# Kernel optimization log

Measured on AMD Instinct MI355X. Metric: run time of the kernel, lower is better.

The kernel has to match this reference:

```python
import jax, jax.numpy as jnp
import numpy as np

B, R, S, H = 4, 64, 512, 768
E = 64            # candidate entities per example
SEG = 128         # seg_emb_dim
NT, NC, NP = 6, 13, 3
REP = 3 * H + 2 * SEG  # rel_rep_size = 2560
NEG = -1e30


def setup_inputs() -> dict:
    key = jax.random.key(0)
    ks = jax.random.split(key, 12)
    hidden_states = jax.random.normal(ks[0], (B, S, H), dtype=jnp.float32)
    rel_pairs = jax.random.randint(ks[1], (B, R, 2), 0, E, dtype=jnp.int64)
    rel_masks = jax.random.randint(ks[2], (B, R, S), 0, 2, dtype=jnp.int32)
    rel_sizes = jax.random.randint(ks[3], (B, R, 2), 0, 30, dtype=jnp.int64)
    ent_span_reps = jax.random.normal(ks[4], (B, E, H), dtype=jnp.float32)
    ent_segs_embs = jax.random.normal(ks[5], (B, E, SEG), dtype=jnp.float32)
    s = 1.0 / np.sqrt(REP)
    W_type = jax.random.uniform(ks[6], (REP, NT), jnp.float32, -s, s)
    b_type = jax.random.uniform(ks[7], (NT,), jnp.float32, -s, s)
    W_cate = jax.random.uniform(ks[8], (REP, NC), jnp.float32, -s, s)
    b_cate = jax.random.uniform(ks[9], (NC,), jnp.float32, -s, s)
    W_pola = jax.random.uniform(ks[10], (REP, NP), jnp.float32, -s, s)
    b_pola = jax.random.uniform(ks[11], (NP,), jnp.float32, -s, s)
    return {"hidden_states": hidden_states, "rel_pairs": rel_pairs,
            "rel_masks": rel_masks, "rel_sizes": rel_sizes,
            "ent_span_reps": ent_span_reps, "ent_segs_embs": ent_segs_embs,
            "W_type": W_type, "b_type": b_type, "W_cate": W_cate,
            "b_cate": b_cate, "W_pola": W_pola, "b_pola": b_pola}


def reference(hidden_states, rel_pairs, rel_masks, rel_sizes,
              ent_span_reps, ent_segs_embs,
              W_type, b_type, W_cate, b_cate, W_pola, b_pola):
    batch, max_rels, _ = rel_pairs.shape
    # batched gather: ent_span_reps[b, rel_pairs[b]] -> [B, R, 2, H] -> [B, R, 2H]
    pair_span = jnp.take_along_axis(
        ent_span_reps[:, :, None, :],
        rel_pairs[:, None, :, :, None].reshape(batch, max_rels * 2, 1, 1), axis=1
    ).reshape(batch, max_rels, -1)
    pair_segs = jnp.take_along_axis(
        ent_segs_embs[:, :, None, :],
        rel_pairs[:, None, :, :, None].reshape(batch, max_rels * 2, 1, 1), axis=1
    ).reshape(batch, max_rels, -1)
    # masked max over seq: scores [B, R, S, H]
    mask_add = (rel_masks == 0).astype(jnp.float32) * NEG          # [B, R, S]
    ctx = jnp.max(hidden_states[:, None, :, :] + mask_add[..., None], axis=2)  # [B, R, H]
    has_ctx = jnp.any(rel_masks != 0, axis=-1)                      # [B, R]
    ctx = jnp.where(has_ctx[..., None], ctx, 0.0)
    features = jnp.concatenate([pair_span, pair_segs, ctx], axis=2)  # [B, R, 2560]
    # dropout is identity at inference
    rel_type_logits = features @ W_type + b_type
    rel_cate_logits = features @ W_cate + b_cate
    rel_pola_logits = features @ W_pola + b_pola
    return (rel_type_logits, rel_cate_logits, rel_pola_logits)
```

## Files before the change

### kernel.cpp

```cpp
#include <hip/hip_runtime.h>
#include <math.h>

#define BB 4
#define RR 64
#define SS 512
#define HH 768
#define EE 64
#define SEGD 128
#define NT 6
#define NC 13
#define NP 3
#define NO (NT + NC + NP)
#define REP 2560
#define RPG 8
#define NGRP (RR / RPG)
#define NEGV -1e30f

__global__ __launch_bounds__(256)
void p1_maxctx(const float* __restrict__ hidden,
               const int*   __restrict__ rel_masks,
               float* __restrict__ ws,
               int SC)
{
    const int bid  = blockIdx.x;
    const int sc   = bid % SC;
    const int grp  = (bid / SC) % NGRP;
    const int b    = bid / (SC * NGRP);
    const int t    = threadIdx.x;
    const int rows = SS / SC;
    const int s0   = sc * rows;
    const int r0   = grp * RPG;

    __shared__ float sadd[RPG * SS];

    for (int i = t; i < RPG * rows; i += 256) {
        const int r = i / rows;
        const int s = i - r * rows;
        const int mv = rel_masks[((size_t)(b * RR + r0 + r)) * SS + s0 + s];
        sadd[r * rows + s] = mv ? 0.f : NEGV;
    }
    __syncthreads();

    float m[RPG][3];
#pragma unroll
    for (int r = 0; r < RPG; ++r) { m[r][0] = -INFINITY; m[r][1] = -INFINITY; m[r][2] = -INFINITY; }

#pragma unroll 2
    for (int s = 0; s < rows; ++s) {
        const float* hp = hidden + ((size_t)(b * SS + s0 + s)) * HH;
        const float v0 = hp[t];
        const float v1 = hp[t + 256];
        const float v2 = hp[t + 512];
#pragma unroll
        for (int r = 0; r < RPG; ++r) {
            const float a = sadd[r * rows + s];
            m[r][0] = fmaxf(m[r][0], v0 + a);
            m[r][1] = fmaxf(m[r][1], v1 + a);
            m[r][2] = fmaxf(m[r][2], v2 + a);
        }
    }

#pragma unroll
    for (int r = 0; r < RPG; ++r) {
        float* wp = ws + (((size_t)(b * RR + r0 + r) * SC) + sc) * HH;
        wp[t]       = m[r][0];
        wp[t + 256] = m[r][1];
        wp[t + 512] = m[r][2];
    }
}

__global__ __launch_bounds__(256)
void p2_head(const float* __restrict__ ws,
             const int*   __restrict__ rel_pairs,
             const float* __restrict__ span,
             const float* __restrict__ segs,
             const float* __restrict__ Wt, const float* __restrict__ bt,
             const float* __restrict__ Wc, const float* __restrict__ bc,
             const float* __restrict__ Wp, const float* __restrict__ bp,
             float* __restrict__ out, int SC)
{
    const int br = blockIdx.x;
    const int b  = br / RR;
    const int t  = threadIdx.x;

    __shared__ float feat[REP];
    __shared__ float red[4][NO];

    const int i0 = rel_pairs[(size_t)br * 2 + 0];
    const int i1 = rel_pairs[(size_t)br * 2 + 1];
    const float* sp0 = span + ((size_t)b * EE + i0) * HH;
    const float* sp1 = span + ((size_t)b * EE + i1) * HH;
    feat[t]            = sp0[t];
    feat[t + 256]      = sp0[t + 256];
    feat[t + 512]      = sp0[t + 512];
    feat[HH + t]       = sp1[t];
    feat[HH + t + 256] = sp1[t + 256];
    feat[HH + t + 512] = sp1[t + 512];
    const float* sg0 = segs + ((size_t)b * EE + i0) * SEGD;
    const float* sg1 = segs + ((size_t)b * EE + i1) * SEGD;
    if (t < SEGD) feat[2 * HH + t] = sg0[t];
    else          feat[2 * HH + SEGD + (t - SEGD)] = sg1[t - SEGD];

    float m0 = -INFINITY, m1 = -INFINITY, m2 = -INFINITY;
    for (int c = 0; c < SC; ++c) {
        const float* wp = ws + ((size_t)br * SC + c) * HH;
        m0 = fmaxf(m0, wp[t]);
        m1 = fmaxf(m1, wp[t + 256]);
        m2 = fmaxf(m2, wp[t + 512]);
    }
    if (m0 < -1e29f) m0 = 0.f;
    if (m1 < -1e29f) m1 = 0.f;
    if (m2 < -1e29f) m2 = 0.f;
    const int CTX0 = 2 * HH + 2 * SEGD;
    feat[CTX0 + t]       = m0;
    feat[CTX0 + t + 256] = m1;
    feat[CTX0 + t + 512] = m2;
    __syncthreads();

    float acc[NO];
#pragma unroll
    for (int o = 0; o < NO; ++o) acc[o] = 0.f;
    for (int f = t; f < REP; f += 256) {
        const float fv = feat[f];
        const float* wt = Wt + (size_t)f * NT;
        const float* wc = Wc + (size_t)f * NC;
        const float* wp = Wp + (size_t)f * NP;
#pragma unroll
        for (int o = 0; o < NT; ++o) acc[o]           += fv * wt[o];
#pragma unroll
        for (int o = 0; o < NC; ++o) acc[NT + o]      += fv * wc[o];
#pragma unroll
        for (int o = 0; o < NP; ++o) acc[NT + NC + o] += fv * wp[o];
    }
#pragma unroll
    for (int o = 0; o < NO; ++o) {
#pragma unroll
        for (int off = 32; off > 0; off >>= 1)
            acc[o] += __shfl_down(acc[o], off, 64);
    }
    const int wid  = t >> 6;
    const int lane = t & 63;
    if (lane == 0) {
#pragma unroll
        for (int o = 0; o < NO; ++o) red[wid][o] = acc[o];
    }
    __syncthreads();

    if (t < NO) {
        const float v = red[0][t] + red[1][t] + red[2][t] + red[3][t];
        if (t < NT) {
            out[(size_t)br * NT + t] = v + bt[t];
        } else if (t < NT + NC) {
            const int o = t - NT;
            out[(size_t)BB * RR * NT + (size_t)br * NC + o] = v + bc[o];
        } else {
            const int o = t - NT - NC;
            out[(size_t)BB * RR * (NT + NC) + (size_t)br * NP + o] = v + bp[o];
        }
    }
}

__global__ __launch_bounds__(256)
void rel_cls_fused(const float* __restrict__ hidden,
                   const int*   __restrict__ rel_pairs,
                   const int*   __restrict__ rel_masks,
                   const float* __restrict__ span,
                   const float* __restrict__ segs,
                   const float* __restrict__ Wt, const float* __restrict__ bt,
                   const float* __restrict__ Wc, const float* __restrict__ bc,
                   const float* __restrict__ Wp, const float* __restrict__ bp,
                   float* __restrict__ out)
{
    const int br = blockIdx.x;
    const int b  = br / RR;
    const int t  = threadIdx.x;

    __shared__ float sadd[SS];
    __shared__ float feat[REP];
    __shared__ float red[4][NO];

    const int* mrow = rel_masks + (size_t)br * SS;
    sadd[t]       = mrow[t] ? 0.f : NEGV;
    sadd[t + 256] = mrow[t + 256] ? 0.f : NEGV;

    const int i0 = rel_pairs[(size_t)br * 2 + 0];
    const int i1 = rel_pairs[(size_t)br * 2 + 1];
    const float* sp0 = span + ((size_t)b * EE + i0) * HH;
    const float* sp1 = span + ((size_t)b * EE + i1) * HH;
    feat[t]            = sp0[t];
    feat[t + 256]      = sp0[t + 256];
    feat[t + 512]      = sp0[t + 512];
    feat[HH + t]       = sp1[t];
    feat[HH + t + 256] = sp1[t + 256];
    feat[HH + t + 512] = sp1[t + 512];
    const float* sg0 = segs + ((size_t)b * EE + i0) * SEGD;
    const float* sg1 = segs + ((size_t)b * EE + i1) * SEGD;
    if (t < SEGD) feat[2 * HH + t] = sg0[t];
    else          feat[2 * HH + SEGD + (t - SEGD)] = sg1[t - SEGD];
    __syncthreads();

    float m0 = -INFINITY, m1 = -INFINITY, m2 = -INFINITY;
#pragma unroll 4
    for (int s = 0; s < SS; ++s) {
        const float* hp = hidden + ((size_t)b * SS + s) * HH;
        const float a = sadd[s];
        m0 = fmaxf(m0, hp[t] + a);
        m1 = fmaxf(m1, hp[t + 256] + a);
        m2 = fmaxf(m2, hp[t + 512] + a);
    }
    if (m0 < -1e29f) m0 = 0.f;
    if (m1 < -1e29f) m1 = 0.f;
    if (m2 < -1e29f) m2 = 0.f;
    const int CTX0 = 2 * HH + 2 * SEGD;
    feat[CTX0 + t]       = m0;
    feat[CTX0 + t + 256] = m1;
    feat[CTX0 + t + 512] = m2;
    __syncthreads();

    float acc[NO];
#pragma unroll
    for (int o = 0; o < NO; ++o) acc[o] = 0.f;
    for (int f = t; f < REP; f += 256) {
        const float fv = feat[f];
        const float* wt = Wt + (size_t)f * NT;
        const float* wc = Wc + (size_t)f * NC;
        const float* wp = Wp + (size_t)f * NP;
#pragma unroll
        for (int o = 0; o < NT; ++o) acc[o]           += fv * wt[o];
#pragma unroll
        for (int o = 0; o < NC; ++o) acc[NT + o]      += fv * wc[o];
#pragma unroll
        for (int o = 0; o < NP; ++o) acc[NT + NC + o] += fv * wp[o];
    }
#pragma unroll
    for (int o = 0; o < NO; ++o) {
#pragma unroll
        for (int off = 32; off > 0; off >>= 1)
            acc[o] += __shfl_down(acc[o], off, 64);
    }
    const int wid  = t >> 6;
    const int lane = t & 63;
    if (lane == 0) {
#pragma unroll
        for (int o = 0; o < NO; ++o) red[wid][o] = acc[o];
    }
    __syncthreads();

    if (t < NO) {
        const float v = red[0][t] + red[1][t] + red[2][t] + red[3][t];
        if (t < NT) {
            out[(size_t)br * NT + t] = v + bt[t];
        } else if (t < NT + NC) {
            const int o = t - NT;
            out[(size_t)BB * RR * NT + (size_t)br * NC + o] = v + bc[o];
        } else {
            const int o = t - NT - NC;
            out[(size_t)BB * RR * (NT + NC) + (size_t)br * NP + o] = v + bp[o];
        }
    }
}

extern "C" void kernel_launch(void* const* d_in, const int* in_sizes, int n_in,
                              void* d_out, int out_size, void* d_ws, size_t ws_size,
                              hipStream_t stream) {
    const float* hidden = (const float*)d_in[0];
    const int*   pairs  = (const int*)d_in[1];
    const int*   masks  = (const int*)d_in[2];
    const float* span   = (const float*)d_in[4];
    const float* segs   = (const float*)d_in[5];
    const float* Wt     = (const float*)d_in[6];
    const float* bt     = (const float*)d_in[7];
    const float* Wc     = (const float*)d_in[8];
    const float* bc     = (const float*)d_in[9];
    const float* Wp     = (const float*)d_in[10];
    const float* bp     = (const float*)d_in[11];
    float* out = (float*)d_out;

    const size_t slot = (size_t)BB * RR * HH * sizeof(float);
    int SC = 0;
    for (int c = 16; c >= 1; c >>= 1) {
        if ((size_t)c * slot <= ws_size) { SC = c; break; }
    }

    if (SC >= 1) {
        float* ws = (float*)d_ws;
        dim3 g1(BB * NGRP * SC), blk(256);
        hipLaunchKernelGGL(p1_maxctx, g1, blk, 0, stream, hidden, masks, ws, SC);
        dim3 g2(BB * RR);
        hipLaunchKernelGGL(p2_head, g2, blk, 0, stream, ws, pairs, span, segs,
                           Wt, bt, Wc, bc, Wp, bp, out, SC);
    } else {
        dim3 grid(BB * RR), blk(256);
        hipLaunchKernelGGL(rel_cls_fused, grid, blk, 0, stream,
                           hidden, pairs, masks, span, segs,
                           Wt, bt, Wc, bc, Wp, bp, out);
    }
}
```

Before: 28.39 us.

## Retile masked-max pass: all 64 relations per block over 8-wide hidden slices

The first pass changes its split. Each block now covers one batch, an 8-column slice of the hidden dimension and a quarter of the sequence, with one thread per relation and each wave taking 32 rows. Hidden values are read with float4 loads, and the mask is kept as bytes in shared memory, so each hidden element is loaded once per block for all 64 relations instead of once per group of 8. Partial maxima from the four waves are reduced in shared memory, and the sequence split is fixed at 4 chunks. This cuts repeated hidden-state reads and the per-relation register pressure, at the cost of many narrow 32-byte accesses per row and a strided ws write pattern.

```diff
diff --git a/kernel.cpp b/kernel.cpp
--- a/kernel.cpp
+++ b/kernel.cpp
@@ -12,60 +12,75 @@
 #define NP 3
 #define NO (NT + NC + NP)
 #define REP 2560
-#define RPG 8
-#define NGRP (RR / RPG)
 #define NEGV -1e30f
 
-__global__ __launch_bounds__(256)
-void p1_maxctx(const float* __restrict__ hidden,
-               const int*   __restrict__ rel_masks,
-               float* __restrict__ ws,
-               int SC)
+#define HC 8
+#define NHB (HH / HC)
+#define SCP 4
+#define SROWS (SS / SCP)
+#define NB1 (BB * NHB * SCP)
+#define PART_ELEMS ((size_t)BB * RR * SCP * HH)
+
+__global__ __launch_bounds__(256, 6)
+void p1_ctx(const float* __restrict__ hidden,
+            const int*   __restrict__ rel_masks,
+            float* __restrict__ ws)
 {
-    const int bid  = blockIdx.x;
-    const int sc   = bid % SC;
-    const int grp  = (bid / SC) % NGRP;
-    const int b    = bid / (SC * NGRP);
-    const int t    = threadIdx.x;
-    const int rows = SS / SC;
-    const int s0   = sc * rows;
-    const int r0   = grp * RPG;
-
-    __shared__ float sadd[RPG * SS];
-
-    for (int i = t; i < RPG * rows; i += 256) {
-        const int r = i / rows;
-        const int s = i - r * rows;
-        const int mv = rel_masks[((size_t)(b * RR + r0 + r)) * SS + s0 + s];
-        sadd[r * rows + s] = mv ? 0.f : NEGV;
-    }
-    __syncthreads();
-
-    float m[RPG][3];
-#pragma unroll
-    for (int r = 0; r < RPG; ++r) { m[r][0] = -INFINITY; m[r][1] = -INFINITY; m[r][2] = -INFINITY; }
-
-#pragma unroll 2
-    for (int s = 0; s < rows; ++s) {
-        const float* hp = hidden + ((size_t)(b * SS + s0 + s)) * HH;
-        const float v0 = hp[t];
-        const float v1 = hp[t + 256];
-        const float v2 = hp[t + 512];
-#pragma unroll
-        for (int r = 0; r < RPG; ++r) {
-            const float a = sadd[r * rows + s];
-            m[r][0] = fmaxf(m[r][0], v0 + a);
-            m[r][1] = fmaxf(m[r][1], v1 + a);
-            m[r][2] = fmaxf(m[r][2], v2 + a);
+    const int bid = blockIdx.x;
+    const int sc  = bid & 3;
+    const int hc  = (bid >> 2) % NHB;
+    const int b   = bid / (4 * NHB);
+    const int t   = threadIdx.x;
+    const int w   = t >> 6;
+    const int r   = t & 63;
+    const int h0  = hc * HC;
+    const int s0  = sc * SROWS;
+
+    __shared__ unsigned char keep[64 * 132];
+    __shared__ float part[4 * 64 * 9];
+
+    const int mbase = b * RR * SS + s0;
+    for (int k = t; k < 64 * SROWS; k += 256) {
+        const int rr = k >> 7;
+        const int s  = k & 127;
+        keep[rr * 132 + s] = (unsigned char)(rel_masks[(size_t)mbase + rr * SS + s] != 0);
+    }
+    __syncthreads();
+
+    float a0 = -INFINITY, a1 = -INFINITY, a2 = -INFINITY, a3 = -INFINITY;
+    float a4 = -INFINITY, a5 = -INFINITY, a6 = -INFINITY, a7 = -INFINITY;
+    const float* hp = hidden + ((size_t)b * SS + s0 + w * 32) * HH + h0;
+    const unsigned char* kp = &keep[r * 132 + w * 32];
+#pragma unroll 4
+    for (int s = 0; s < 32; ++s) {
+        const float4 va = *reinterpret_cast<const float4*>(hp + (size_t)s * HH);
+        const float4 vb = *reinterpret_cast<const float4*>(hp + (size_t)s * HH + 4);
+        const float a = kp[s] ? 0.f : NEGV;
+        a0 = fmaxf(a0, va.x + a);
+        a1 = fmaxf(a1, va.y + a);
+        a2 = fmaxf(a2, va.z + a);
+        a3 = fmaxf(a3, va.w + a);
+        a4 = fmaxf(a4, vb.x + a);
+        a5 = fmaxf(a5, vb.y + a);
+        a6 = fmaxf(a6, vb.z + a);
+        a7 = fmaxf(a7, vb.w + a);
+    }
+
+    float* pp = &part[(w * 64 + r) * 9];
+    pp[0] = a0; pp[1] = a1; pp[2] = a2; pp[3] = a3;
+    pp[4] = a4; pp[5] = a5; pp[6] = a6; pp[7] = a7;
+    __syncthreads();
+
+    if (w == 0) {
+        float* wp = ws + (((size_t)(b * RR + r)) * SCP + sc) * HH + h0;
+#pragma unroll
+        for (int j = 0; j < 8; ++j) {
+            float v = part[(0 * 64 + r) * 9 + j];
+            v = fmaxf(v, part[(1 * 64 + r) * 9 + j]);
+            v = fmaxf(v, part[(2 * 64 + r) * 9 + j]);
+            v = fmaxf(v, part[(3 * 64 + r) * 9 + j]);
+            wp[j] = v;
         }
-    }
-
-#pragma unroll
-    for (int r = 0; r < RPG; ++r) {
-        float* wp = ws + (((size_t)(b * RR + r0 + r) * SC) + sc) * HH;
-        wp[t]       = m[r][0];
-        wp[t + 256] = m[r][1];
-        wp[t + 512] = m[r][2];
     }
 }
 
@@ -77,7 +92,7 @@
              const float* __restrict__ Wt, const float* __restrict__ bt,
              const float* __restrict__ Wc, const float* __restrict__ bc,
              const float* __restrict__ Wp, const float* __restrict__ bp,
-             float* __restrict__ out, int SC)
+             float* __restrict__ out)
 {
     const int br = blockIdx.x;
     const int b  = br / RR;
@@ -85,6 +100,106 @@
 
     __shared__ float feat[REP];
     __shared__ float red[4][NO];
+
+    const int i0 = rel_pairs[(size_t)br * 2 + 0];
+    const int i1 = rel_pairs[(size_t)br * 2 + 1];
+
+    const float* sp0 = span + ((size_t)b * EE + i0) * HH;
+    const float* sp1 = span + ((size_t)b * EE + i1) * HH;
+    feat[t]            = sp0[t];
+    feat[t + 256]      = sp0[t + 256];
+    feat[t + 512]      = sp0[t + 512];
+    feat[HH + t]       = sp1[t];
+    feat[HH + t + 256] = sp1[t + 256];
+    feat[HH + t + 512] = sp1[t + 512];
+    const float* sg0 = segs + ((size_t)b * EE + i0) * SEGD;
+    const float* sg1 = segs + ((size_t)b * EE + i1) * SEGD;
+    if (t < SEGD) feat[2 * HH + t] = sg0[t];
+    else          feat[2 * HH + SEGD + (t - SEGD)] = sg1[t - SEGD];
+
+    const float* wbase = ws + (size_t)br * SCP * HH;
+    float m0 = -INFINITY, m1 = -INFINITY, m2 = -INFINITY;
+#pragma unroll
+    for (int c = 0; c < SCP; ++c) {
+        const float* wp = wbase + (size_t)c * HH;
+        m0 = fmaxf(m0, wp[t]);
+        m1 = fmaxf(m1, wp[t + 256]);
+        m2 = fmaxf(m2, wp[t + 512]);
+    }
+    if (m0 < -1e29f) m0 = 0.f;
+    if (m1 < -1e29f) m1 = 0.f;
+    if (m2 < -1e29f) m2 = 0.f;
+    const int CTX0 = 2 * HH + 2 * SEGD;
+    feat[CTX0 + t]       = m0;
+    feat[CTX0 + t + 256] = m1;
+    feat[CTX0 + t + 512] = m2;
+    __syncthreads();
+
+    float acc[NO];
+#pragma unroll
+    for (int o = 0; o < NO; ++o) acc[o] = 0.f;
+    for (int f = t; f < REP; f += 256) {
+        const float fv = feat[f];
+        const float* wt = Wt + (size_t)f * NT;
+        const float* wc = Wc + (size_t)f * NC;
+        const float* wp = Wp + (size_t)f * NP;
+#pragma unroll
+        for (int o = 0; o < NT; ++o) acc[o]           += fv * wt[o];
+#pragma unroll
+        for (int o = 0; o < NC; ++o) acc[NT + o]      += fv * wc[o];
+#pragma unroll
+        for (int o = 0; o < NP; ++o) acc[NT + NC + o] += fv * wp[o];
+    }
+#pragma unroll
+    for (int o = 0; o < NO; ++o) {
+#pragma unroll
+        for (int off = 32; off > 0; off >>= 1)
+            acc[o] += __shfl_down(acc[o], off, 64);
+    }
+    const int wid  = t >> 6;
+    const int lane = t & 63;
+    if (lane == 0) {
+#pragma unroll
+        for (int o = 0; o < NO; ++o) red[wid][o] = acc[o];
+    }
+    __syncthreads();
+
+    if (t < NO) {
+        const float v = red[0][t] + red[1][t] + red[2][t] + red[3][t];
+        if (t < NT) {
+            out[(size_t)br * NT + t] = v + bt[t];
+        } else if (t < NT + NC) {
+            const int o = t - NT;
+            out[(size_t)BB * RR * NT + (size_t)br * NC + o] = v + bc[o];
+        } else {
+            const int o = t - NT - NC;
+            out[(size_t)BB * RR * (NT + NC) + (size_t)br * NP + o] = v + bp[o];
+        }
+    }
+}
+
+__global__ __launch_bounds__(256)
+void rel_cls_fused(const float* __restrict__ hidden,
+                   const int*   __restrict__ rel_pairs,
+                   const int*   __restrict__ rel_masks,
+                   const float* __restrict__ span,
+                   const float* __restrict__ segs,
+                   const float* __restrict__ Wt, const float* __restrict__ bt,
+                   const float* __restrict__ Wc, const float* __restrict__ bc,
+                   const float* __restrict__ Wp, const float* __restrict__ bp,
+                   float* __restrict__ out)
+{
+    const int br = blockIdx.x;
+    const int b  = br / RR;
+    const int t  = threadIdx.x;
+
+    __shared__ float sadd[SS];
+    __shared__ float feat[REP];
+    __shared__ float red[4][NO];
+
+    const int* mrow = rel_masks + (size_t)br * SS;
+    sadd[t]       = mrow[t] ? 0.f : NEGV;
+    sadd[t + 256] = mrow[t + 256] ? 0.f : NEGV;
 
     const int i0 = rel_pairs[(size_t)br * 2 + 0];
     const int i1 = rel_pairs[(size_t)br * 2 + 1];
@@ -100,107 +215,10 @@
     const float* sg1 = segs + ((size_t)b * EE + i1) * SEGD;
     if (t < SEGD) feat[2 * HH + t] = sg0[t];
     else          feat[2 * HH + SEGD + (t - SEGD)] = sg1[t - SEGD];
+    __syncthreads();
 
     float m0 = -INFINITY, m1 = -INFINITY, m2 = -INFINITY;
-    for (int c = 0; c < SC; ++c) {
-        const float* wp = ws + ((size_t)br * SC + c) * HH;
-        m0 = fmaxf(m0, wp[t]);
-        m1 = fmaxf(m1, wp[t + 256]);
-        m2 = fmaxf(m2, wp[t + 512]);
-    }
-    if (m0 < -1e29f) m0 = 0.f;
-    if (m1 < -1e29f) m1 = 0.f;
-    if (m2 < -1e29f) m2 = 0.f;
-    const int CTX0 = 2 * HH + 2 * SEGD;
-    feat[CTX0 + t]       = m0;
-    feat[CTX0 + t + 256] = m1;
-    feat[CTX0 + t + 512] = m2;
-    __syncthreads();
-
-    float acc[NO];
-#pragma unroll
-    for (int o = 0; o < NO; ++o) acc[o] = 0.f;
-    for (int f = t; f < REP; f += 256) {
-        const float fv = feat[f];
-        const float* wt = Wt + (size_t)f * NT;
-        const float* wc = Wc + (size_t)f * NC;
-        const float* wp = Wp + (size_t)f * NP;
-#pragma unroll
-        for (int o = 0; o < NT; ++o) acc[o]           += fv * wt[o];
-#pragma unroll
-        for (int o = 0; o < NC; ++o) acc[NT + o]      += fv * wc[o];
-#pragma unroll
-        for (int o = 0; o < NP; ++o) acc[NT + NC + o] += fv * wp[o];
-    }
-#pragma unroll
-    for (int o = 0; o < NO; ++o) {
-#pragma unroll
-        for (int off = 32; off > 0; off >>= 1)
-            acc[o] += __shfl_down(acc[o], off, 64);
-    }
-    const int wid  = t >> 6;
-    const int lane = t & 63;
-    if (lane == 0) {
-#pragma unroll
-        for (int o = 0; o < NO; ++o) red[wid][o] = acc[o];
-    }
-    __syncthreads();
-
-    if (t < NO) {
-        const float v = red[0][t] + red[1][t] + red[2][t] + red[3][t];
-        if (t < NT) {
-            out[(size_t)br * NT + t] = v + bt[t];
-        } else if (t < NT + NC) {
-            const int o = t - NT;
-            out[(size_t)BB * RR * NT + (size_t)br * NC + o] = v + bc[o];
-        } else {
-            const int o = t - NT - NC;
-            out[(size_t)BB * RR * (NT + NC) + (size_t)br * NP + o] = v + bp[o];
-        }
-    }
-}
-
-__global__ __launch_bounds__(256)
-void rel_cls_fused(const float* __restrict__ hidden,
-                   const int*   __restrict__ rel_pairs,
-                   const int*   __restrict__ rel_masks,
-                   const float* __restrict__ span,
-                   const float* __restrict__ segs,
-                   const float* __restrict__ Wt, const float* __restrict__ bt,
-                   const float* __restrict__ Wc, const float* __restrict__ bc,
-                   const float* __restrict__ Wp, const float* __restrict__ bp,
-                   float* __restrict__ out)
-{
-    const int br = blockIdx.x;
-    const int b  = br / RR;
-    const int t  = threadIdx.x;
-
-    __shared__ float sadd[SS];
-    __shared__ float feat[REP];
-    __shared__ float red[4][NO];
-
-    const int* mrow = rel_masks + (size_t)br * SS;
-    sadd[t]       = mrow[t] ? 0.f : NEGV;
-    sadd[t + 256] = mrow[t + 256] ? 0.f : NEGV;
-
-    const int i0 = rel_pairs[(size_t)br * 2 + 0];
-    const int i1 = rel_pairs[(size_t)br * 2 + 1];
-    const float* sp0 = span + ((size_t)b * EE + i0) * HH;
-    const float* sp1 = span + ((size_t)b * EE + i1) * HH;
-    feat[t]            = sp0[t];
-    feat[t + 256]      = sp0[t + 256];
-    feat[t + 512]      = sp0[t + 512];
-    feat[HH + t]       = sp1[t];
-    feat[HH + t + 256] = sp1[t + 256];
-    feat[HH + t + 512] = sp1[t + 512];
-    const float* sg0 = segs + ((size_t)b * EE + i0) * SEGD;
-    const float* sg1 = segs + ((size_t)b * EE + i1) * SEGD;
-    if (t < SEGD) feat[2 * HH + t] = sg0[t];
-    else          feat[2 * HH + SEGD + (t - SEGD)] = sg1[t - SEGD];
-    __syncthreads();
-
-    float m0 = -INFINITY, m1 = -INFINITY, m2 = -INFINITY;
-#pragma unroll 4
+#pragma unroll 8
     for (int s = 0; s < SS; ++s) {
         const float* hp = hidden + ((size_t)b * SS + s) * HH;
         const float a = sadd[s];
@@ -275,23 +293,15 @@
     const float* Wp     = (const float*)d_in[10];
     const float* bp     = (const float*)d_in[11];
     float* out = (float*)d_out;
-
-    const size_t slot = (size_t)BB * RR * HH * sizeof(float);
-    int SC = 0;
-    for (int c = 16; c >= 1; c >>= 1) {
-        if ((size_t)c * slot <= ws_size) { SC = c; break; }
-    }
-
-    if (SC >= 1) {
-        float* ws = (float*)d_ws;
-        dim3 g1(BB * NGRP * SC), blk(256);
-        hipLaunchKernelGGL(p1_maxctx, g1, blk, 0, stream, hidden, masks, ws, SC);
-        dim3 g2(BB * RR);
-        hipLaunchKernelGGL(p2_head, g2, blk, 0, stream, ws, pairs, span, segs,
-                           Wt, bt, Wc, bc, Wp, bp, out, SC);
+    float* ws  = (float*)d_ws;
+
+    if (ws_size >= PART_ELEMS * sizeof(float)) {
+        hipLaunchKernelGGL(p1_ctx, dim3(NB1), dim3(256), 0, stream,
+                           hidden, masks, ws);
+        hipLaunchKernelGGL(p2_head, dim3(BB * RR), dim3(256), 0, stream,
+                           ws, pairs, span, segs, Wt, bt, Wc, bc, Wp, bp, out);
     } else {
-        dim3 grid(BB * RR), blk(256);
-        hipLaunchKernelGGL(rel_cls_fused, grid, blk, 0, stream,
+        hipLaunchKernelGGL(rel_cls_fused, dim3(BB * RR), dim3(256), 0, stream,
                            hidden, pairs, masks, span, segs,
                            Wt, bt, Wc, bc, Wp, bp, out);
     }
```

Result: faster. 27.27 us (median of 2 runs) (-3.9%).
